# Kernel optimization log

Hardware: AMD Instinct MI355X
Metric: run time of the kernel (lower is better)

## Reference

```python
import jax, jax.numpy as jnp
import numpy as np

N = 100000
E = 1600000
IN_FEATS = 512
H1, F1 = 8, 8          # layer1: 8 heads x 8 units
H2, F2 = 1, 40         # layer2: 1 head x out_feats
NEG_SLOPE = 0.2


def setup_inputs() -> dict:
    key = jax.random.key(0)
    ks = jax.random.split(key, 12)
    x = jax.random.normal(ks[0], (N, IN_FEATS), dtype=jnp.float32)
    src = jax.random.randint(ks[1], (E,), 0, N, dtype=jnp.int32)
    dst = jax.random.randint(ks[2], (E,), 0, N, dtype=jnp.int32)
    # Xavier-ish init for params
    W1 = jax.random.normal(ks[3], (IN_FEATS, H1 * F1), dtype=jnp.float32) * (1.0 / np.sqrt(IN_FEATS))
    al1 = jax.random.normal(ks[4], (H1, F1), dtype=jnp.float32) * 0.1
    ar1 = jax.random.normal(ks[5], (H1, F1), dtype=jnp.float32) * 0.1
    b1 = jnp.zeros((H1 * F1,), dtype=jnp.float32)
    W2 = jax.random.normal(ks[6], (H1 * F1, H2 * F2), dtype=jnp.float32) * (1.0 / np.sqrt(H1 * F1))
    al2 = jax.random.normal(ks[7], (H2, F2), dtype=jnp.float32) * 0.1
    ar2 = jax.random.normal(ks[8], (H2, F2), dtype=jnp.float32) * 0.1
    b2 = jnp.zeros((H2 * F2,), dtype=jnp.float32)
    return {"x": x, "src": src, "dst": dst,
            "W1": W1, "al1": al1, "ar1": ar1, "b1": b1,
            "W2": W2, "al2": al2, "ar2": ar2, "b2": b2}


def _gat_conv(feat, src, dst, W, al, ar, b, activation):
    """DGL-style GATConv (dropout disabled / eval mode)."""
    n = feat.shape[0]
    heads, fdim = al.shape
    h = (feat @ W).reshape(n, heads, fdim)            # [N, H, F]
    el = jnp.einsum('nhf,hf->nh', h, al)              # [N, H]
    er = jnp.einsum('nhf,hf->nh', h, ar)              # [N, H]
    e = jax.nn.leaky_relu(el[src] + er[dst], NEG_SLOPE)   # [E, H]
    # edge softmax over incoming edges of each dst node (numerically stable)
    m = jax.ops.segment_max(e, dst, num_segments=n)   # [N, H]
    ex = jnp.exp(e - m[dst])
    s = jax.ops.segment_sum(ex, dst, num_segments=n)  # [N, H]
    alpha = ex / s[dst]                               # [E, H]
    msg = h[src] * alpha[:, :, None]                  # [E, H, F]
    rst = jax.ops.segment_sum(msg, dst, num_segments=n)  # [N, H, F]
    rst = rst + b.reshape(1, heads, fdim)
    if activation is not None:
        rst = activation(rst)
    return rst


def reference(x, src, dst, W1, al1, ar1, b1, W2, al2, ar2, b2):
    h1 = _gat_conv(x, src, dst, W1, al1, ar1, b1, jax.nn.elu)   # [N, H1, F1]
    h1 = h1.reshape(x.shape[0], H1 * F1)                        # flatten(1)
    h2 = _gat_conv(h1, src, dst, W2, al2, ar2, b2, None)        # [N, 1, F2]
    logits = h2.mean(axis=1)                                    # [N, F2]
    return jax.nn.log_softmax(logits, axis=1)
```

## Files before the change

### kernel.cpp

```cpp
#include <hip/hip_runtime.h>
#include <cstdint>
#include <cstddef>

#define IN_F 512
#define C1 64
#define NH 8
#define FD 8
#define C2 40
#define NEG 0.2f

typedef __attribute__((ext_vector_type(8))) short bf16x8;
typedef __attribute__((ext_vector_type(4))) float f32x4;

__device__ inline unsigned short f32_to_bf16_rne(float f) {
    unsigned int u = __float_as_uint(f);
    unsigned int r = (u + 0x7FFFu + ((u >> 16) & 1u)) >> 16;
    return (unsigned short)r;
}
__device__ inline float bf16_to_f32(unsigned short s) {
    return __uint_as_float(((unsigned int)s) << 16);
}

__global__ __launch_bounds__(256) void hist_pre_k(const int* __restrict__ dst, int* __restrict__ deg,
                                                  int* __restrict__ pos, int E, int HB,
                                                  const float* __restrict__ W1, const float* __restrict__ W2,
                                                  unsigned short* __restrict__ wt_hi, unsigned short* __restrict__ wt_lo,
                                                  unsigned short* __restrict__ w2t_hi, unsigned short* __restrict__ w2t_lo) {
    if ((int)blockIdx.x < HB) {
        int base = blockIdx.x * 1024 + threadIdx.x;
#pragma unroll
        for (int j = 0; j < 4; j++) {
            int e = base + j * 256;
            if (e < E) pos[e] = atomicAdd(&deg[dst[e]], 1);
        }
        return;
    }
    int id = (blockIdx.x - HB) * 256 + threadIdx.x;
    if (id < IN_F * C1) {
        int col = id & (C1 - 1);
        int k = id >> 6;
        float w = W1[id];
        unsigned short hb = f32_to_bf16_rne(w);
        unsigned short lb = f32_to_bf16_rne(w - bf16_to_f32(hb));
        wt_hi[(size_t)col * IN_F + k] = hb;
        wt_lo[(size_t)col * IN_F + k] = lb;
    } else {
        int id2 = id - IN_F * C1;
        if (id2 < 48 * 64) {
            int c = id2 >> 6, k = id2 & 63;
            float w = (c < C2) ? W2[(size_t)k * C2 + c] : 0.f;
            unsigned short hb = f32_to_bf16_rne(w);
            unsigned short lb = f32_to_bf16_rne(w - bf16_to_f32(hb));
            w2t_hi[c * 64 + k] = hb;
            w2t_lo[c * 64 + k] = lb;
        }
    }
}

__global__ __launch_bounds__(1024) void scan_local_k(const int* __restrict__ deg, int* __restrict__ rowp,
                                                     int* __restrict__ bsums, int n) {
    __shared__ int tmp[1024];
    int tx = threadIdx.x;
    int i = blockIdx.x * 1024 + tx;
    int v = (i < n) ? deg[i] : 0;
    tmp[tx] = v;
    __syncthreads();
    for (int d = 1; d < 1024; d <<= 1) {
        int t = (tx >= d) ? tmp[tx - d] : 0;
        __syncthreads();
        tmp[tx] += t;
        __syncthreads();
    }
    if (i < n) rowp[i] = tmp[tx] - v;
    if (tx == 1023) bsums[blockIdx.x] = tmp[tx];
}

__global__ __launch_bounds__(1024) void scan_add_k(int* rowp, const int* __restrict__ bsums, int n, int nb) {
    __shared__ int red[128];
    int tx = threadIdx.x;
    if (tx < 128) red[tx] = (tx < blockIdx.x && tx < nb) ? bsums[tx] : 0;
    __syncthreads();
    if (tx < 64) red[tx] += red[tx + 64];
    __syncthreads();
    if (tx < 32) red[tx] += red[tx + 32];
    __syncthreads();
    if (tx < 16) red[tx] += red[tx + 16];
    __syncthreads();
    if (tx < 8) red[tx] += red[tx + 8];
    __syncthreads();
    if (tx < 4) red[tx] += red[tx + 4];
    __syncthreads();
    if (tx < 2) red[tx] += red[tx + 2];
    __syncthreads();
    if (tx == 0) red[0] += red[1];
    __syncthreads();
    int off = red[0];
    int i = blockIdx.x * 1024 + tx;
    if (i < n) rowp[i] += off;
}

__global__ __launch_bounds__(256) void scat_gemm1_k(const int* __restrict__ src, const int* __restrict__ dst,
                                                    const int* __restrict__ rowp, const int* __restrict__ pos,
                                                    int* __restrict__ csr_src, int E, int SB,
                                                    const float* __restrict__ x,
                                                    const unsigned short* __restrict__ wt_hi,
                                                    const unsigned short* __restrict__ wt_lo,
                                                    const float* __restrict__ al, const float* __restrict__ ar,
                                                    unsigned short* __restrict__ hb_out,
                                                    float* __restrict__ el, float* __restrict__ er, int N) {
    __shared__ alignas(16) unsigned short wlds[2][8192];
    if ((int)blockIdx.x < SB) {
        int base = blockIdx.x * 1024 + threadIdx.x;
#pragma unroll
        for (int j = 0; j < 4; j++) {
            int e = base + j * 256;
            if (e < E) csr_src[rowp[dst[e]] + pos[e]] = src[e];
        }
        return;
    }
    const int gb = blockIdx.x - SB;
    const int tid = threadIdx.x;
    const int wave = tid >> 6, lane = tid & 63;
    const int m = lane & 15, q = lane >> 4;
    const int row = gb * 64 + wave * 16 + m;
    const int row_c = row < N ? row : N - 1;
    const float* xp = x + (size_t)row_c * IN_F + q * 8;

    f32x4 acc[4];
#pragma unroll
    for (int ct = 0; ct < 4; ct++) acc[ct] = (f32x4){0.f, 0.f, 0.f, 0.f};
    float4 xr[2][4];

#define WLOAD(c, buf)                                                                              \
    {                                                                                              \
        _Pragma("unroll") for (int j_ = 0; j_ < 4; j_++) {                                         \
            int slot_ = j_ * 256 + wave * 64 + lane;                                               \
            const unsigned short* gbase_ = (slot_ < 512) ? wt_hi : wt_lo;                          \
            int s_ = slot_ & 511;                                                                  \
            int col_ = s_ & 63, kq_ = s_ >> 6;                                                     \
            const unsigned short* g_ = gbase_ + (size_t)col_ * IN_F + (c) * 64 + kq_ * 8;          \
            unsigned short* l_ = &wlds[buf][0] + (size_t)(j_ * 256 + wave * 64) * 8;               \
            __builtin_amdgcn_global_load_lds((const __attribute__((address_space(1))) unsigned int*)g_, \
                                             (__attribute__((address_space(3))) unsigned int*)l_,  \
                                             16, 0, 0);                                            \
        }                                                                                          \
    }
#define XLOAD(c, r)                                  \
    {                                                \
        const float* xsrc_ = xp + (c) * 64;          \
        (r)[0] = *(const float4*)(xsrc_);            \
        (r)[1] = *(const float4*)(xsrc_ + 4);        \
        (r)[2] = *(const float4*)(xsrc_ + 32);       \
        (r)[3] = *(const float4*)(xsrc_ + 36);       \
    }

    WLOAD(0, 0);
    XLOAD(0, xr[0]);

    for (int c = 0; c < 8; c++) {
        int p = c & 1;
        __syncthreads();
        if (c < 7) {
            WLOAD(c + 1, p ^ 1);
            XLOAD(c + 1, xr[p ^ 1]);
        }
#pragma unroll
        for (int ki = 0; ki < 2; ki++) {
            float f[8];
            f[0] = xr[p][ki * 2].x; f[1] = xr[p][ki * 2].y; f[2] = xr[p][ki * 2].z; f[3] = xr[p][ki * 2].w;
            f[4] = xr[p][ki * 2 + 1].x; f[5] = xr[p][ki * 2 + 1].y; f[6] = xr[p][ki * 2 + 1].z; f[7] = xr[p][ki * 2 + 1].w;
            unsigned int u[8], lu[8];
#pragma unroll
            for (int j = 0; j < 8; j++) u[j] = __float_as_uint(f[j]);
            union { uint4 u4; bf16x8 v; } H, L;
            H.u4.x = __builtin_amdgcn_perm(u[1], u[0], 0x07060302u);
            H.u4.y = __builtin_amdgcn_perm(u[3], u[2], 0x07060302u);
            H.u4.z = __builtin_amdgcn_perm(u[5], u[4], 0x07060302u);
            H.u4.w = __builtin_amdgcn_perm(u[7], u[6], 0x07060302u);
#pragma unroll
            for (int j = 0; j < 8; j++)
                lu[j] = __float_as_uint(f[j] - __uint_as_float(u[j] & 0xFFFF0000u));
            L.u4.x = __builtin_amdgcn_perm(lu[1], lu[0], 0x07060302u);
            L.u4.y = __builtin_amdgcn_perm(lu[3], lu[2], 0x07060302u);
            L.u4.z = __builtin_amdgcn_perm(lu[5], lu[4], 0x07060302u);
            L.u4.w = __builtin_amdgcn_perm(lu[7], lu[6], 0x07060302u);
            int kq = ki * 4 + q;
#pragma unroll
            for (int ct = 0; ct < 4; ct++) {
                int slot = kq * 64 + ct * 16 + m;
                bf16x8 bh = *(const bf16x8*)&wlds[p][slot * 8];
                bf16x8 bl = *(const bf16x8*)&wlds[p][4096 + slot * 8];
                acc[ct] = __builtin_amdgcn_mfma_f32_16x16x32_bf16(H.v, bh, acc[ct], 0, 0, 0);
                acc[ct] = __builtin_amdgcn_mfma_f32_16x16x32_bf16(L.v, bh, acc[ct], 0, 0, 0);
                acc[ct] = __builtin_amdgcn_mfma_f32_16x16x32_bf16(H.v, bl, acc[ct], 0, 0, 0);
            }
        }
    }
    int rbase = gb * 64 + wave * 16 + q * 4;
#pragma unroll
    for (int r = 0; r < 4; r++) {
        int ro = rbase + r;
        if (ro < N) {
#pragma unroll
            for (int ct = 0; ct < 4; ct++)
                hb_out[(size_t)ro * C1 + ct * 16 + m] = f32_to_bf16_rne(acc[ct][r]);
        }
    }

    __syncthreads();
    float* hst = (float*)&wlds[0][0];
    {
        int rr = wave * 16 + q * 4;
#pragma unroll
        for (int r = 0; r < 4; r++)
#pragma unroll
            for (int ct = 0; ct < 4; ct++)
                hst[(rr + r) * 69 + ct * 16 + m] = acc[ct][r];
    }
    __syncthreads();
    for (int id = tid; id < 512; id += 256) {
        int r = id >> 3, hd = id & 7;
        int nn = gb * 64 + r;
        if (nn < N) {
            float e_l = 0.f, e_r = 0.f;
#pragma unroll
            for (int f = 0; f < 8; f++) {
                float v = hst[r * 69 + hd * 8 + f];
                e_l += v * al[hd * 8 + f];
                e_r += v * ar[hd * 8 + f];
            }
            el[(size_t)nn * NH + hd] = e_l;
            er[(size_t)nn * NH + hd] = e_r;
        }
    }
#undef WLOAD
#undef XLOAD
}

__global__ __launch_bounds__(256) void l1_wave_k(const unsigned short* __restrict__ hb,
                                                 const float* __restrict__ el, const float* __restrict__ er,
                                                 const int* __restrict__ rowp, const int* __restrict__ deg,
                                                 const int* __restrict__ csr_src, const float* __restrict__ b1,
                                                 float* __restrict__ h1out, int N) {
    int n = (blockIdx.x * 256 + threadIdx.x) >> 6;
    if (n >= N) return;
    int lane = threadIdx.x & 63;
    int q = lane >> 4;
    int f = lane & 15;
    int hd = f >> 1;
    int start = rowp[n], cnt = deg[n];
    float erd = er[(size_t)n * NH + hd];
    const uint2* hb64 = (const uint2*)hb;
    const int* cp = csr_src + start;
    float a0 = 0.f, a1 = 0.f, a2 = 0.f, a3 = 0.f, s = 0.f;
    if (cnt > 0) {
        int lastc = cnt - 1;
        int c0 = cp[(q < cnt) ? q : lastc];
        int c1 = cp[(4 + q < cnt) ? 4 + q : lastc];
        int i = 0;
        while (i + 8 < cnt) {
            int i8 = i + 8;
            int c2 = cp[(i8 + q < cnt) ? i8 + q : lastc];
            int c3 = cp[(i8 + 4 + q < cnt) ? i8 + 4 + q : lastc];
            float e0 = el[(size_t)c0 * NH + hd] + erd;
            float e1 = el[(size_t)c1 * NH + hd] + erd;
            uint2 v0 = hb64[(size_t)c0 * 16 + f];
            uint2 v1 = hb64[(size_t)c1 * 16 + f];
            e0 = e0 > 0.f ? e0 : NEG * e0;
            e1 = e1 > 0.f ? e1 : NEG * e1;
            float w0 = __expf(e0), w1 = __expf(e1);
            s += w0 + w1;
            a0 += w0 * __uint_as_float(v0.x << 16) + w1 * __uint_as_float(v1.x << 16);
            a1 += w0 * __uint_as_float(v0.x & 0xFFFF0000u) + w1 * __uint_as_float(v1.x & 0xFFFF0000u);
            a2 += w0 * __uint_as_float(v0.y << 16) + w1 * __uint_as_float(v1.y << 16);
            a3 += w0 * __uint_as_float(v0.y & 0xFFFF0000u) + w1 * __uint_as_float(v1.y & 0xFFFF0000u);
            c0 = c2; c1 = c3; i = i8;
        }
        {
            bool m0 = (i + q) < cnt, m1 = (i + 4 + q) < cnt;
            float e0 = el[(size_t)c0 * NH + hd] + erd;
            float e1 = el[(size_t)c1 * NH + hd] + erd;
            uint2 v0 = hb64[(size_t)c0 * 16 + f];
            uint2 v1 = hb64[(size_t)c1 * 16 + f];
            e0 = e0 > 0.f ? e0 : NEG * e0;
            e1 = e1 > 0.f ? e1 : NEG * e1;
            float w0 = m0 ? __expf(e0) : 0.f;
            float w1 = m1 ? __expf(e1) : 0.f;
            s += w0 + w1;
            a0 += w0 * __uint_as_float(v0.x << 16) + w1 * __uint_as_float(v1.x << 16);
            a1 += w0 * __uint_as_float(v0.x & 0xFFFF0000u) + w1 * __uint_as_float(v1.x & 0xFFFF0000u);
            a2 += w0 * __uint_as_float(v0.y << 16) + w1 * __uint_as_float(v1.y << 16);
            a3 += w0 * __uint_as_float(v0.y & 0xFFFF0000u) + w1 * __uint_as_float(v1.y & 0xFFFF0000u);
        }
    }
    a0 += __shfl_xor(a0, 16); a0 += __shfl_xor(a0, 32);
    a1 += __shfl_xor(a1, 16); a1 += __shfl_xor(a1, 32);
    a2 += __shfl_xor(a2, 16); a2 += __shfl_xor(a2, 32);
    a3 += __shfl_xor(a3, 16); a3 += __shfl_xor(a3, 32);
    s  += __shfl_xor(s, 16);  s  += __shfl_xor(s, 32);
    float sinv = (s > 0.f) ? 1.f / s : 0.f;
    float4 bv = *(const float4*)(b1 + f * 4);
    float o0 = a0 * sinv + bv.x;
    float o1 = a1 * sinv + bv.y;
    float o2 = a2 * sinv + bv.z;
    float o3 = a3 * sinv + bv.w;
    o0 = o0 > 0.f ? o0 : (__expf(o0) - 1.f);
    o1 = o1 > 0.f ? o1 : (__expf(o1) - 1.f);
    o2 = o2 > 0.f ? o2 : (__expf(o2) - 1.f);
    o3 = o3 > 0.f ? o3 : (__expf(o3) - 1.f);
    if (q == 0) *(float4*)(h1out + (size_t)n * C1 + f * 4) = make_float4(o0, o1, o2, o3);
}

__global__ __launch_bounds__(256) void gemm2_attn2_k(const float* __restrict__ h1,
                                                     const unsigned short* __restrict__ w2t_hi,
                                                     const unsigned short* __restrict__ w2t_lo,
                                                     const float* __restrict__ al2, const float* __restrict__ ar2,
                                                     unsigned short* __restrict__ h2b, float* __restrict__ el2,
                                                     float* __restrict__ er2, int N) {
    __shared__ float h2s[64][49];
    __shared__ float a2s[2 * C2];
    int t = threadIdx.x;
    int wave = t >> 6, lane = t & 63;
    int m = lane & 15, q = lane >> 4;
    int n0 = blockIdx.x * 64;
    if (t < C2) a2s[t] = al2[t];
    else if (t < 2 * C2) a2s[t] = ar2[t - C2];
    int row = n0 + wave * 16 + m;
    int row_c = row < N ? row : N - 1;
    const float* hp = h1 + (size_t)row_c * C1 + q * 8;
    f32x4 acc[3];
#pragma unroll
    for (int ct = 0; ct < 3; ct++) acc[ct] = (f32x4){0.f, 0.f, 0.f, 0.f};
#pragma unroll
    for (int ks = 0; ks < 2; ks++) {
        float4 r0 = *(const float4*)(hp + ks * 32);
        float4 r1 = *(const float4*)(hp + ks * 32 + 4);
        float f[8];
        f[0] = r0.x; f[1] = r0.y; f[2] = r0.z; f[3] = r0.w;
        f[4] = r1.x; f[5] = r1.y; f[6] = r1.z; f[7] = r1.w;
        unsigned int u[8], lu[8];
#pragma unroll
        for (int j = 0; j < 8; j++) u[j] = __float_as_uint(f[j]);
        union { uint4 u4; bf16x8 v; } H, L;
        H.u4.x = __builtin_amdgcn_perm(u[1], u[0], 0x07060302u);
        H.u4.y = __builtin_amdgcn_perm(u[3], u[2], 0x07060302u);
        H.u4.z = __builtin_amdgcn_perm(u[5], u[4], 0x07060302u);
        H.u4.w = __builtin_amdgcn_perm(u[7], u[6], 0x07060302u);
#pragma unroll
        for (int j = 0; j < 8; j++)
            lu[j] = __float_as_uint(f[j] - __uint_as_float(u[j] & 0xFFFF0000u));
        L.u4.x = __builtin_amdgcn_perm(lu[1], lu[0], 0x07060302u);
        L.u4.y = __builtin_amdgcn_perm(lu[3], lu[2], 0x07060302u);
        L.u4.z = __builtin_amdgcn_perm(lu[5], lu[4], 0x07060302u);
        L.u4.w = __builtin_amdgcn_perm(lu[7], lu[6], 0x07060302u);
        int kb = ks * 32 + q * 8;
#pragma unroll
        for (int ct = 0; ct < 3; ct++) {
            int col = ct * 16 + m;
            bf16x8 bh = *(const bf16x8*)(w2t_hi + col * 64 + kb);
            bf16x8 bl = *(const bf16x8*)(w2t_lo + col * 64 + kb);
            acc[ct] = __builtin_amdgcn_mfma_f32_16x16x32_bf16(H.v, bh, acc[ct], 0, 0, 0);
            acc[ct] = __builtin_amdgcn_mfma_f32_16x16x32_bf16(L.v, bh, acc[ct], 0, 0, 0);
            acc[ct] = __builtin_amdgcn_mfma_f32_16x16x32_bf16(H.v, bl, acc[ct], 0, 0, 0);
        }
    }
    int rl = wave * 16 + q * 4;
#pragma unroll
    for (int ct = 0; ct < 3; ct++)
#pragma unroll
        for (int r = 0; r < 4; r++) h2s[rl + r][ct * 16 + m] = acc[ct][r];
    __syncthreads();
    unsigned int* h2d = (unsigned int*)h2b;
    for (int o = t; o < 64 * 20; o += 256) {
        int r = o / 20, cd = o % 20;
        int nn = n0 + r;
        if (nn < N) {
            unsigned int lo16 = f32_to_bf16_rne(h2s[r][cd * 2]);
            unsigned int hi16 = f32_to_bf16_rne(h2s[r][cd * 2 + 1]);
            h2d[(size_t)nn * 20 + cd] = lo16 | (hi16 << 16);
        }
    }
    if (t < 64) {
        int nn = n0 + t;
        if (nn < N) {
            float e_l = 0.f, e_r = 0.f;
#pragma unroll
            for (int c = 0; c < C2; c++) {
                float v = h2s[t][c];
                e_l += v * a2s[c];
                e_r += v * a2s[C2 + c];
            }
            el2[nn] = e_l;
            er2[nn] = e_r;
        }
    }
}

__global__ __launch_bounds__(256) void l2_fused_k(const unsigned short* __restrict__ h2b,
                                                  const float* __restrict__ el, const float* __restrict__ er,
                                                  const int* __restrict__ rowp, const int* __restrict__ deg,
                                                  const int* __restrict__ csr_src, const float* __restrict__ b2,
                                                  float* __restrict__ out, int N) {
    int tid = threadIdx.x;
    int n = blockIdx.x * 32 + (tid >> 3);
    int sub = tid & 7;
    if (n >= N) return;
    float vals[8];
    if (sub < 5) {
        int start = rowp[n], cnt = deg[n];
        float erd = er[n];
        float s = 0.f;
        float acc[8];
#pragma unroll
        for (int j = 0; j < 8; j++) acc[j] = 0.f;
        const int* cp = csr_src + start;
        if (cnt > 0) {
            int last = cnt - 1;
            int c0 = cp[0];
            int c1 = cp[1 < cnt ? 1 : last];
            int c2 = cp[2 < cnt ? 2 : last];
            int c3 = cp[3 < cnt ? 3 : last];
            int i = 0;
            while (i + 4 < cnt) {
                int i4 = i + 4;
                int p0 = cp[i4];
                int p1 = cp[(i4 + 1 < cnt) ? i4 + 1 : last];
                int p2 = cp[(i4 + 2 < cnt) ? i4 + 2 : last];
                int p3 = cp[(i4 + 3 < cnt) ? i4 + 3 : last];
                float e0 = el[c0], e1 = el[c1], e2 = el[c2], e3 = el[c3];
                bf16x8 v0 = *(const bf16x8*)(h2b + (size_t)c0 * C2 + sub * 8);
                bf16x8 v1 = *(const bf16x8*)(h2b + (size_t)c1 * C2 + sub * 8);
                bf16x8 v2 = *(const bf16x8*)(h2b + (size_t)c2 * C2 + sub * 8);
                bf16x8 v3 = *(const bf16x8*)(h2b + (size_t)c3 * C2 + sub * 8);
                e0 += erd; e1 += erd; e2 += erd; e3 += erd;
                e0 = e0 > 0.f ? e0 : NEG * e0;
                e1 = e1 > 0.f ? e1 : NEG * e1;
                e2 = e2 > 0.f ? e2 : NEG * e2;
                e3 = e3 > 0.f ? e3 : NEG * e3;
                float w0 = __expf(e0), w1 = __expf(e1), w2 = __expf(e2), w3 = __expf(e3);
                s += (w0 + w1) + (w2 + w3);
#pragma unroll
                for (int j = 0; j < 8; j++) {
                    acc[j] += w0 * bf16_to_f32((unsigned short)v0[j]) + w1 * bf16_to_f32((unsigned short)v1[j]) +
                              w2 * bf16_to_f32((unsigned short)v2[j]) + w3 * bf16_to_f32((unsigned short)v3[j]);
                }
                c0 = p0; c1 = p1; c2 = p2; c3 = p3; i = i4;
            }
            {
                bool m0 = i < cnt, m1 = i + 1 < cnt, m2 = i + 2 < cnt, m3 = i + 3 < cnt;
                float e0 = el[c0], e1 = el[c1], e2 = el[c2], e3 = el[c3];
                bf16x8 v0 = *(const bf16x8*)(h2b + (size_t)c0 * C2 + sub * 8);
                bf16x8 v1 = *(const bf16x8*)(h2b + (size_t)c1 * C2 + sub * 8);
                bf16x8 v2 = *(const bf16x8*)(h2b + (size_t)c2 * C2 + sub * 8);
                bf16x8 v3 = *(const bf16x8*)(h2b + (size_t)c3 * C2 + sub * 8);
                e0 += erd; e1 += erd; e2 += erd; e3 += erd;
                e0 = e0 > 0.f ? e0 : NEG * e0;
                e1 = e1 > 0.f ? e1 : NEG * e1;
                e2 = e2 > 0.f ? e2 : NEG * e2;
                e3 = e3 > 0.f ? e3 : NEG * e3;
                float w0 = m0 ? __expf(e0) : 0.f;
                float w1 = m1 ? __expf(e1) : 0.f;
                float w2 = m2 ? __expf(e2) : 0.f;
                float w3 = m3 ? __expf(e3) : 0.f;
                s += (w0 + w1) + (w2 + w3);
#pragma unroll
                for (int j = 0; j < 8; j++) {
                    acc[j] += w0 * bf16_to_f32((unsigned short)v0[j]) + w1 * bf16_to_f32((unsigned short)v1[j]) +
                              w2 * bf16_to_f32((unsigned short)v2[j]) + w3 * bf16_to_f32((unsigned short)v3[j]);
                }
            }
        }
        float sinv = (s > 0.f) ? 1.f / s : 0.f;
        const float* bp = b2 + sub * 8;
#pragma unroll
        for (int j = 0; j < 8; j++) vals[j] = acc[j] * sinv + bp[j];
    } else {
#pragma unroll
        for (int j = 0; j < 8; j++) vals[j] = -1e30f;
    }
    float mx = vals[0];
#pragma unroll
    for (int j = 1; j < 8; j++) mx = fmaxf(mx, vals[j]);
#pragma unroll
    for (int off = 1; off < 8; off <<= 1) mx = fmaxf(mx, __shfl_xor(mx, off, 8));
    float se = 0.f;
#pragma unroll
    for (int j = 0; j < 8; j++) se += __expf(vals[j] - mx);
#pragma unroll
    for (int off = 1; off < 8; off <<= 1) se += __shfl_xor(se, off, 8);
    float ls = __logf(se) + mx;
    if (sub < 5) {
        float* op = out + (size_t)n * C2 + sub * 8;
        *(float4*)(op) = make_float4(vals[0] - ls, vals[1] - ls, vals[2] - ls, vals[3] - ls);
        *(float4*)(op + 4) = make_float4(vals[4] - ls, vals[5] - ls, vals[6] - ls, vals[7] - ls);
    }
}

extern "C" void kernel_launch(void* const* d_in, const int* in_sizes, int n_in,
                              void* d_out, int out_size, void* d_ws, size_t ws_size,
                              hipStream_t stream) {
    (void)n_in; (void)out_size; (void)ws_size;
    const float* x   = (const float*)d_in[0];
    const int*   src = (const int*)d_in[1];
    const int*   dst = (const int*)d_in[2];
    const float* W1  = (const float*)d_in[3];
    const float* al1 = (const float*)d_in[4];
    const float* ar1 = (const float*)d_in[5];
    const float* b1  = (const float*)d_in[6];
    const float* W2  = (const float*)d_in[7];
    const float* al2 = (const float*)d_in[8];
    const float* ar2 = (const float*)d_in[9];
    const float* b2  = (const float*)d_in[10];
    float* out = (float*)d_out;
    const int N = in_sizes[0] / IN_F;
    const int E = in_sizes[1];

    char* w = (char*)d_ws;
    auto alloc = [&](size_t bytes) -> char* {
        char* p = w;
        w += (bytes + 255) & ~(size_t)255;
        return p;
    };
    int* deg     = (int*)alloc((size_t)N * 4);
    int* rowp    = (int*)alloc((size_t)N * 4);
    int* bsums   = (int*)alloc(512);
    int* pos     = (int*)alloc((size_t)E * 4);
    int* csr_src = (int*)alloc((size_t)E * 4);
    unsigned short* wt_hi = (unsigned short*)alloc((size_t)IN_F * C1 * 2);
    unsigned short* wt_lo = (unsigned short*)alloc((size_t)IN_F * C1 * 2);
    unsigned short* w2t_hi = (unsigned short*)alloc((size_t)48 * 64 * 2);
    unsigned short* w2t_lo = (unsigned short*)alloc((size_t)48 * 64 * 2);
    unsigned short* hb    = (unsigned short*)alloc((size_t)N * C1 * 2);
    float* el1   = (float*)alloc((size_t)N * NH * 4);
    float* er1   = (float*)alloc((size_t)N * NH * 4);
    float* h1    = (float*)alloc((size_t)N * C1 * 4);
    unsigned short* h2b = (unsigned short*)alloc((size_t)N * C2 * 2);
    float* el2   = (float*)alloc((size_t)N * 4);
    float* er2   = (float*)alloc((size_t)N * 4);

    hipMemsetAsync(deg, 0, (size_t)N * 4, stream);

    int HB = (E + 1023) / 1024;
    int PREB = (IN_F * C1 + 48 * 64 + 255) / 256;
    int GB = (N + 63) / 64;
    int nb = (N + 1023) / 1024;

    hist_pre_k<<<HB + PREB, 256, 0, stream>>>(dst, deg, pos, E, HB, W1, W2, wt_hi, wt_lo, w2t_hi, w2t_lo);
    scan_local_k<<<nb, 1024, 0, stream>>>(deg, rowp, bsums, N);
    scan_add_k<<<nb, 1024, 0, stream>>>(rowp, bsums, N, nb);
    scat_gemm1_k<<<HB + GB, 256, 0, stream>>>(src, dst, rowp, pos, csr_src, E, HB,
                                              x, wt_hi, wt_lo, al1, ar1, hb, el1, er1, N);
    l1_wave_k<<<(N * 64 + 255) / 256, 256, 0, stream>>>(hb, el1, er1, rowp, deg, csr_src, b1, h1, N);
    gemm2_attn2_k<<<GB, 256, 0, stream>>>(h1, w2t_hi, w2t_lo, al2, ar2, h2b, el2, er2, N);
    l2_fused_k<<<(N + 31) / 32, 256, 0, stream>>>(h2b, el2, er2, rowp, deg, csr_src, b2, out, N);
}
```

Baseline: 544.8 us.

## Build CSR via two-level bucketed counting sort instead of per-edge global atomics

```diff
diff --git a/kernel.cpp b/kernel.cpp
--- a/kernel.cpp
+++ b/kernel.cpp
@@ -21,17 +21,17 @@
     return __uint_as_float(((unsigned int)s) << 16);
 }
 
-__global__ __launch_bounds__(256) void hist_pre_k(const int* __restrict__ dst, int* __restrict__ deg,
-                                                  int* __restrict__ pos, int E, int HB,
-                                                  const float* __restrict__ W1, const float* __restrict__ W2,
-                                                  unsigned short* __restrict__ wt_hi, unsigned short* __restrict__ wt_lo,
-                                                  unsigned short* __restrict__ w2t_hi, unsigned short* __restrict__ w2t_lo) {
+__global__ __launch_bounds__(256) void bcount_pre_k(const int* __restrict__ dst, int* __restrict__ bcnt_pad,
+                                                    int E, int HB,
+                                                    const float* __restrict__ W1, const float* __restrict__ W2,
+                                                    unsigned short* __restrict__ wt_hi, unsigned short* __restrict__ wt_lo,
+                                                    unsigned short* __restrict__ w2t_hi, unsigned short* __restrict__ w2t_lo) {
     if ((int)blockIdx.x < HB) {
         int base = blockIdx.x * 1024 + threadIdx.x;
 #pragma unroll
         for (int j = 0; j < 4; j++) {
             int e = base + j * 256;
-            if (e < E) pos[e] = atomicAdd(&deg[dst[e]], 1);
+            if (e < E) atomicAdd(&bcnt_pad[(dst[e] >> 5) * 16], 1);
         }
         return;
     }
@@ -57,6 +57,32 @@
     }
 }
 
+__global__ __launch_bounds__(1024) void bscan_k(const int* __restrict__ bcnt_pad, int* __restrict__ boff,
+                                                int* __restrict__ bcur_pad, int K) {
+    __shared__ int tmp[1024];
+    __shared__ int carry;
+    int tx = threadIdx.x;
+    if (tx == 0) carry = 0;
+    __syncthreads();
+    for (int base = 0; base < K; base += 1024) {
+        int idx = base + tx;
+        int v = (idx < K) ? bcnt_pad[idx * 16] : 0;
+        tmp[tx] = v;
+        __syncthreads();
+        for (int d = 1; d < 1024; d <<= 1) {
+            int t = (tx >= d) ? tmp[tx - d] : 0;
+            __syncthreads();
+            tmp[tx] += t;
+            __syncthreads();
+        }
+        int excl = tmp[tx] - v + carry;
+        if (idx < K) { boff[idx] = excl; bcur_pad[idx * 16] = excl; }
+        __syncthreads();
+        if (tx == 1023) carry += tmp[1023];
+        __syncthreads();
+    }
+}
+
 __global__ __launch_bounds__(1024) void scan_local_k(const int* __restrict__ deg, int* __restrict__ rowp,
                                                      int* __restrict__ bsums, int n) {
     __shared__ int tmp[1024];
@@ -99,22 +125,74 @@
     if (i < n) rowp[i] += off;
 }
 
-__global__ __launch_bounds__(256) void scat_gemm1_k(const int* __restrict__ src, const int* __restrict__ dst,
-                                                    const int* __restrict__ rowp, const int* __restrict__ pos,
-                                                    int* __restrict__ csr_src, int E, int SB,
-                                                    const float* __restrict__ x,
-                                                    const unsigned short* __restrict__ wt_hi,
-                                                    const unsigned short* __restrict__ wt_lo,
-                                                    const float* __restrict__ al, const float* __restrict__ ar,
-                                                    unsigned short* __restrict__ hb_out,
-                                                    float* __restrict__ el, float* __restrict__ er, int N) {
+__global__ __launch_bounds__(256) void bdeg_k(const uint2* __restrict__ staging, const int* __restrict__ boff,
+                                              const int* __restrict__ bcnt_pad, int* __restrict__ deg, int N) {
+    __shared__ int cnt[32];
+    int b = blockIdx.x;
+    int tx = threadIdx.x;
+    if (tx < 32) cnt[tx] = 0;
+    __syncthreads();
+    int start = boff[b], cn = bcnt_pad[b * 16];
+    for (int i = tx; i < cn; i += 256) {
+        uint2 e = staging[start + i];
+        atomicAdd(&cnt[e.y & 31], 1);
+    }
+    __syncthreads();
+    int n = b * 32 + tx;
+    if (tx < 32 && n < N) deg[n] = cnt[tx];
+}
+
+__global__ __launch_bounds__(256) void csr_k(const uint2* __restrict__ staging, const int* __restrict__ boff,
+                                             const int* __restrict__ bcnt_pad, const int* __restrict__ rowp,
+                                             int* __restrict__ csr_src, int N) {
+    __shared__ int cur[32];
+    int b = blockIdx.x;
+    int tx = threadIdx.x;
+    int n = b * 32 + tx;
+    if (tx < 32) cur[tx] = (n < N) ? rowp[n] : 0;
+    __syncthreads();
+    int start = boff[b], cn = bcnt_pad[b * 16];
+    for (int i = tx; i < cn; i += 256) {
+        uint2 e = staging[start + i];
+        int slot = atomicAdd(&cur[e.y & 31], 1);
+        csr_src[slot] = e.x;
+    }
+}
+
+__global__ __launch_bounds__(256) void bplace_gemm1_k(const int* __restrict__ src, const int* __restrict__ dst,
+                                                      int* __restrict__ bcur_pad, uint2* __restrict__ staging,
+                                                      int E, int SB,
+                                                      const float* __restrict__ x,
+                                                      const unsigned short* __restrict__ wt_hi,
+                                                      const unsigned short* __restrict__ wt_lo,
+                                                      const float* __restrict__ al, const float* __restrict__ ar,
+                                                      unsigned short* __restrict__ hb_out,
+                                                      float* __restrict__ el, float* __restrict__ er, int N) {
     __shared__ alignas(16) unsigned short wlds[2][8192];
     if ((int)blockIdx.x < SB) {
         int base = blockIdx.x * 1024 + threadIdx.x;
-#pragma unroll
-        for (int j = 0; j < 4; j++) {
-            int e = base + j * 256;
-            if (e < E) csr_src[rowp[dst[e]] + pos[e]] = src[e];
+        int e3 = base + 768;
+        if (e3 < E) {
+            int d0 = dst[base], d1 = dst[base + 256], d2 = dst[base + 512], d3 = dst[e3];
+            int s0 = src[base], s1 = src[base + 256], s2 = src[base + 512], s3 = src[e3];
+            int p0 = atomicAdd(&bcur_pad[(d0 >> 5) * 16], 1);
+            int p1 = atomicAdd(&bcur_pad[(d1 >> 5) * 16], 1);
+            int p2 = atomicAdd(&bcur_pad[(d2 >> 5) * 16], 1);
+            int p3 = atomicAdd(&bcur_pad[(d3 >> 5) * 16], 1);
+            staging[p0] = make_uint2(s0, d0);
+            staging[p1] = make_uint2(s1, d1);
+            staging[p2] = make_uint2(s2, d2);
+            staging[p3] = make_uint2(s3, d3);
+        } else {
+#pragma unroll
+            for (int j = 0; j < 4; j++) {
+                int e = base + j * 256;
+                if (e < E) {
+                    int d = dst[e];
+                    int p = atomicAdd(&bcur_pad[(d >> 5) * 16], 1);
+                    staging[p] = make_uint2(src[e], d);
+                }
+            }
         }
         return;
     }
@@ -514,6 +592,7 @@
     float* out = (float*)d_out;
     const int N = in_sizes[0] / IN_F;
     const int E = in_sizes[1];
+    const int K = (N + 31) >> 5;
 
     char* w = (char*)d_ws;
     auto alloc = [&](size_t bytes) -> char* {
@@ -521,11 +600,14 @@
         w += (bytes + 255) & ~(size_t)255;
         return p;
     };
-    int* deg     = (int*)alloc((size_t)N * 4);
-    int* rowp    = (int*)alloc((size_t)N * 4);
-    int* bsums   = (int*)alloc(512);
-    int* pos     = (int*)alloc((size_t)E * 4);
-    int* csr_src = (int*)alloc((size_t)E * 4);
+    int* deg      = (int*)alloc((size_t)N * 4);
+    int* rowp     = (int*)alloc((size_t)N * 4);
+    int* bsums    = (int*)alloc(512);
+    int* bcnt_pad = (int*)alloc((size_t)K * 64);
+    int* bcur_pad = (int*)alloc((size_t)K * 64);
+    int* boff     = (int*)alloc((size_t)K * 4);
+    uint2* staging = (uint2*)alloc((size_t)E * 8);
+    int* csr_src  = (int*)alloc((size_t)E * 4);
     unsigned short* wt_hi = (unsigned short*)alloc((size_t)IN_F * C1 * 2);
     unsigned short* wt_lo = (unsigned short*)alloc((size_t)IN_F * C1 * 2);
     unsigned short* w2t_hi = (unsigned short*)alloc((size_t)48 * 64 * 2);
@@ -538,18 +620,21 @@
     float* el2   = (float*)alloc((size_t)N * 4);
     float* er2   = (float*)alloc((size_t)N * 4);
 
-    hipMemsetAsync(deg, 0, (size_t)N * 4, stream);
+    hipMemsetAsync(bcnt_pad, 0, (size_t)K * 64, stream);
 
     int HB = (E + 1023) / 1024;
     int PREB = (IN_F * C1 + 48 * 64 + 255) / 256;
     int GB = (N + 63) / 64;
     int nb = (N + 1023) / 1024;
 
-    hist_pre_k<<<HB + PREB, 256, 0, stream>>>(dst, deg, pos, E, HB, W1, W2, wt_hi, wt_lo, w2t_hi, w2t_lo);
+    bcount_pre_k<<<HB + PREB, 256, 0, stream>>>(dst, bcnt_pad, E, HB, W1, W2, wt_hi, wt_lo, w2t_hi, w2t_lo);
+    bscan_k<<<1, 1024, 0, stream>>>(bcnt_pad, boff, bcur_pad, K);
+    bplace_gemm1_k<<<HB + GB, 256, 0, stream>>>(src, dst, bcur_pad, staging, E, HB,
+                                                x, wt_hi, wt_lo, al1, ar1, hb, el1, er1, N);
+    bdeg_k<<<K, 256, 0, stream>>>(staging, boff, bcnt_pad, deg, N);
     scan_local_k<<<nb, 1024, 0, stream>>>(deg, rowp, bsums, N);
     scan_add_k<<<nb, 1024, 0, stream>>>(rowp, bsums, N, nb);
-    scat_gemm1_k<<<HB + GB, 256, 0, stream>>>(src, dst, rowp, pos, csr_src, E, HB,
-                                              x, wt_hi, wt_lo, al1, ar1, hb, el1, er1, N);
+    csr_k<<<K, 256, 0, stream>>>(staging, boff, bcnt_pad, rowp, csr_src, N);
     l1_wave_k<<<(N * 64 + 255) / 256, 256, 0, stream>>>(hb, el1, er1, rowp, deg, csr_src, b1, h1, N);
     gemm2_attn2_k<<<GB, 256, 0, stream>>>(h1, w2t_hi, w2t_lo, al2, ar2, h2b, el2, er2, N);
     l2_fused_k<<<(N + 31) / 32, 256, 0, stream>>>(h2b, el2, er2, rowp, deg, csr_src, b2, out, N);
```

After: 604.2 us. +10.9%, slower.
